# Optimization experiments

Measured on AMD Instinct MI355X. Metric: run time of the kernel, lower is better.

The kernel has to match this reference:

```python
import jax, jax.numpy as jnp
import numpy as np

N, E, IN = 50000, 800000, 128   # nodes, edges, input feature dim
H, C = 8, 32                    # heads, per-head channels
HC = H * C                      # 256 = concat width
NEG_SLOPE = 0.2
BN_EPS = 1e-5


def _gat_conv(x, src, dst, W, a_src, a_dst, b, heads, out_ch, concat):
    """PyG-style GATConv (eval mode, self-loops already in src/dst)."""
    n = x.shape[0]
    h = (x @ W).reshape(n, heads, out_ch)                 # [N,H,C]
    alpha_s = (h * a_src).sum(-1)                         # [N,H]
    alpha_d = (h * a_dst).sum(-1)                         # [N,H]
    e = jax.nn.leaky_relu(alpha_s[src] + alpha_d[dst], NEG_SLOPE)  # [Etot,H]
    # segment softmax over destination nodes (every node has a self-loop)
    emax = jax.ops.segment_max(e, dst, num_segments=n)    # [N,H]
    e = jnp.exp(e - emax[dst])
    denom = jax.ops.segment_sum(e, dst, num_segments=n)
    alpha = e / (denom[dst] + 1e-16)                      # [Etot,H]
    msg = h[src] * alpha[:, :, None]                      # [Etot,H,C]
    out = jax.ops.segment_sum(msg, dst, num_segments=n)   # [N,H,C]
    out = out.reshape(n, heads * out_ch) if concat else out.mean(axis=1)
    return out + b


def _bn(y, g, beta, m, v):
    return (y - m) * jax.lax.rsqrt(v + BN_EPS) * g + beta


def setup_inputs() -> dict:
    key = jax.random.key(0)
    ks = jax.random.split(key, 32)
    def p(i, shape, s=0.1):
        return jax.random.normal(ks[i], shape, dtype=jnp.float32) * s
    x = jax.random.normal(ks[0], (N, IN), dtype=jnp.float32)
    edge_index = jax.random.randint(ks[1], (2, E), 0, N, dtype=jnp.int32)
    d = dict(
        x=x, edge_index=edge_index,
        W1=p(2, (IN, HC)), a_src1=p(3, (H, C)), a_dst1=p(4, (H, C)), b1=p(5, (HC,)),
        bn1_g=jnp.ones((HC,), jnp.float32), bn1_b=jnp.zeros((HC,), jnp.float32),
        bn1_m=p(6, (HC,)), bn1_v=jax.random.uniform(ks[7], (HC,), jnp.float32, 0.5, 1.5),
        W2=p(8, (HC, HC)), a_src2=p(9, (H, C)), a_dst2=p(10, (H, C)), b2=p(11, (HC,)),
        bn2_g=jnp.ones((HC,), jnp.float32), bn2_b=jnp.zeros((HC,), jnp.float32),
        bn2_m=p(12, (HC,)), bn2_v=jax.random.uniform(ks[13], (HC,), jnp.float32, 0.5, 1.5),
        W3=p(14, (HC, C)), a_src3=p(15, (1, C)), a_dst3=p(16, (1, C)), b3=p(17, (C,)),
        Ws1=p(18, (IN, HC)), bs1=p(19, (HC,)),
        Ws2=p(20, (HC, C)), bs2=p(21, (C,)),
    )
    return d


def reference(x, edge_index, W1, a_src1, a_dst1, b1, bn1_g, bn1_b, bn1_m, bn1_v,
              W2, a_src2, a_dst2, b2, bn2_g, bn2_b, bn2_m, bn2_v,
              W3, a_src3, a_dst3, b3, Ws1, bs1, Ws2, bs2):
    n = x.shape[0]
    loops = jnp.arange(n, dtype=edge_index.dtype)
    src = jnp.concatenate([edge_index[0], loops])   # PyG add_self_loops=True
    dst = jnp.concatenate([edge_index[1], loops])
    x0 = x @ Ws1 + bs1                               # skip1
    h = _gat_conv(x, src, dst, W1, a_src1, a_dst1, b1, H, C, True)
    h = jax.nn.elu(_bn(h, bn1_g, bn1_b, bn1_m, bn1_v)) + x0
    xs = h @ Ws2 + bs2                               # skip2
    h2 = _gat_conv(h, src, dst, W2, a_src2, a_dst2, b2, H, C, True)
    h2 = jax.nn.elu(_bn(h2, bn2_g, bn2_b, bn2_m, bn2_v))
    out = _gat_conv(h2, src, dst, W3, a_src3, a_dst3, b3, 1, C, False) + xs
    return out
```

## Files before the change

### kernel.cpp

```cpp
#include <hip/hip_runtime.h>
#include <hip/hip_bf16.h>

#define NEG_SLOPE 0.2f
#define BN_EPS 1e-5f
#define BSH 8
#define STASH_CAP 6400

typedef __attribute__((ext_vector_type(8))) short bf16x8;
typedef __attribute__((ext_vector_type(4))) float f32x4;
typedef __attribute__((ext_vector_type(2))) float f32x2;

#if defined(__has_builtin)
#if __has_builtin(__builtin_amdgcn_cvt_f32_fp8) && __has_builtin(__builtin_amdgcn_cvt_pk_fp8_f32)
#define HW_FP8 1
#endif
#if __has_builtin(__builtin_amdgcn_cvt_pk_f32_fp8)
#define HW_FP8_PK 1
#endif
#endif

__device__ __forceinline__ float bf2f(unsigned short u) {
    union { unsigned int i; float f; } x;
    x.i = ((unsigned int)u) << 16;
    return x.f;
}
__device__ __forceinline__ unsigned short f2bf(float f) {
    __hip_bfloat16 b = __float2bfloat16(f);
    return *reinterpret_cast<unsigned short*>(&b);
}
__device__ __forceinline__ float lrelu(float v) {
    return v > 0.f ? v : NEG_SLOPE * v;
}

__device__ __forceinline__ unsigned char f8enc(float f) {
#ifdef HW_FP8
    int p = __builtin_amdgcn_cvt_pk_fp8_f32(f, 0.f, 0, false);
    return (unsigned char)(p & 0xff);
#else
    float a = fabsf(f);
    unsigned int sign = (__float_as_uint(f) >> 31) << 7;
    if (a < 0.0009765625f) return (unsigned char)sign;
    a = fminf(a, 448.f);
    unsigned int bits = __float_as_uint(a);
    int e = (int)((bits >> 23) & 0xff) - 127;
    unsigned int mant = bits & 0x7fffff;
    if (e < -6) {
        int q = (int)(a * 512.f + 0.5f);
        if (q >= 8) return (unsigned char)(sign | 0x08);
        return (unsigned char)(sign | q);
    }
    unsigned int m = mant >> 20;
    unsigned int rem = mant & 0xfffff;
    if (rem > 0x80000 || (rem == 0x80000 && (m & 1))) m++;
    if (m == 8) { m = 0; e++; }
    if (e > 8) { e = 8; m = 6; }
    return (unsigned char)(sign | ((unsigned int)(e + 7) << 3) | m);
#endif
}
template <int SEL>
__device__ __forceinline__ float f8dec(unsigned int w) {
#ifdef HW_FP8
    return __builtin_amdgcn_cvt_f32_fp8(w, SEL);
#else
    unsigned int b = (w >> (SEL * 8)) & 0xff;
    unsigned int s = b >> 7, em = b & 0x7f;
    float mag;
    if (em >= 8) {
        unsigned int bits = (((em >> 3) + 120) << 23) | ((em & 7) << 20);
        mag = __uint_as_float(bits);
    } else {
        mag = (float)em * 0.001953125f;
    }
    return s ? -mag : mag;
#endif
}
__device__ __forceinline__ void fma_f8x4(float we, unsigned int wv, float4& acc) {
#ifdef HW_FP8_PK
    f32x2 lo = __builtin_amdgcn_cvt_pk_f32_fp8((int)wv, false);
    f32x2 hi = __builtin_amdgcn_cvt_pk_f32_fp8((int)wv, true);
    acc.x = fmaf(we, lo[0], acc.x);
    acc.y = fmaf(we, lo[1], acc.y);
    acc.z = fmaf(we, hi[0], acc.z);
    acc.w = fmaf(we, hi[1], acc.w);
#else
    acc.x = fmaf(we, f8dec<0>(wv), acc.x);
    acc.y = fmaf(we, f8dec<1>(wv), acc.y);
    acc.z = fmaf(we, f8dec<2>(wv), acc.z);
    acc.w = fmaf(we, f8dec<3>(wv), acc.w);
#endif
}

__device__ __forceinline__ int block_scan_incl(int v, int t) {
    int lane = t & 63, w = t >> 6;
    int sv = v;
    #pragma unroll
    for (int off = 1; off < 64; off <<= 1) {
        int u = __shfl_up(sv, off);
        if (lane >= off) sv += u;
    }
    __shared__ int ws_[4];
    if (lane == 63) ws_[w] = sv;
    __syncthreads();
    if (t == 0) {
        int a = 0;
        #pragma unroll
        for (int k = 0; k < 4; k++) { int x = ws_[k]; ws_[k] = a; a += x; }
    }
    __syncthreads();
    return sv + ws_[w];
}

__global__ __launch_bounds__(256) void phase1(const int* __restrict__ dstl,
                                              int E, int N, int NB,
                                              int* __restrict__ gHist,
                                              const float* __restrict__ x,
                                              unsigned short* __restrict__ xb, int n4x,
                                              const float* __restrict__ W1,
                                              const float* __restrict__ Ws1,
                                              const float* __restrict__ W2,
                                              const float* __restrict__ Ws2,
                                              const float* __restrict__ W3,
                                              const float* __restrict__ a_src1,
                                              const float* __restrict__ a_dst1,
                                              const float* __restrict__ a_src2,
                                              const float* __restrict__ a_dst2,
                                              const float* __restrict__ a_src3,
                                              const float* __restrict__ a_dst3,
                                              unsigned short* __restrict__ Wcat1,
                                              unsigned short* __restrict__ Wcat2,
                                              unsigned short* __restrict__ W3t) {
    int t = threadIdx.x;
    if (blockIdx.x < 256) {
        __shared__ int h[256];
        h[t] = 0;
        __syncthreads();
        int Etot = E + N;
        for (int i = blockIdx.x * 256 + t; i < Etot; i += 256 * 256) {
            int d = (i < E) ? dstl[i] : (i - E);
            atomicAdd(&h[d >> BSH], 1);
        }
        __syncthreads();
        if (t < NB && h[t]) atomicAdd(&gHist[t], h[t]);
        return;
    }
    int i = (blockIdx.x - 256) * 256 + t;
    if (i < n4x) {
        float4 v = reinterpret_cast<const float4*>(x)[i];
        ushort4 o;
        o.x = f2bf(v.x); o.y = f2bf(v.y); o.z = f2bf(v.z); o.w = f2bf(v.w);
        reinterpret_cast<ushort4*>(xb)[i] = o;
        return;
    }
    int j = i - n4x;
    if (j < 32768) {
        int m = j >> 7, k = j & 127;
        Wcat1[j] = f2bf(W1[k * 256 + m]);
    } else if (j < 65536) {
        int q = j - 32768; int m = q >> 7, k = q & 127;
        Wcat1[32768 + q] = f2bf(Ws1[k * 256 + m]);
    } else if (j < 131072) {
        int q = j - 65536; int m = q >> 8, k = q & 255;
        Wcat2[q] = f2bf(W2[k * 256 + m]);
    } else if (j < 139264) {
        int q = j - 131072; int m = q >> 8, k = q & 255;
        Wcat2[65536 + q] = f2bf(Ws2[k * 32 + m]);
    } else if (j < 147456) {
        int q = j - 139264; int m = q >> 8, k = q & 255;
        W3t[q] = f2bf(W3[k * 32 + m]);
    } else if (j < 149504) {
        int q = j - 147456; int r = q >> 7, k = q & 127;
        int h = r & 7;
        const float* av = (r < 8) ? a_src1 : a_dst1;
        float s = 0.f;
        #pragma unroll
        for (int c = 0; c < 32; c++) s += W1[k * 256 + h * 32 + c] * av[h * 32 + c];
        Wcat1[(512 + r) * 128 + k] = f2bf(s);
    } else if (j < 153600) {
        int q = j - 149504; int r = q >> 8, k = q & 255;
        int h = r & 7;
        const float* av = (r < 8) ? a_src2 : a_dst2;
        float s = 0.f;
        #pragma unroll
        for (int c = 0; c < 32; c++) s += W2[k * 256 + h * 32 + c] * av[h * 32 + c];
        Wcat2[(288 + r) * 256 + k] = f2bf(s);
    } else if (j < 154112) {
        int q = j - 153600; int r = q >> 8, k = q & 255;
        const float* av = r ? a_dst3 : a_src3;
        float s = 0.f;
        #pragma unroll
        for (int c = 0; c < 32; c++) s += W3[k * 32 + c] * av[c];
        W3t[(32 + r) * 256 + k] = f2bf(s);
    }
}

__global__ __launch_bounds__(256) void bucket_scatter(const int* __restrict__ srcl,
                                                      const int* __restrict__ dstl,
                                                      int E, int N, int NB,
                                                      const int* __restrict__ gHist,
                                                      int* __restrict__ gCursor,
                                                      unsigned int* __restrict__ bktEdges) {
    __shared__ unsigned int stage[4096];
    __shared__ int lbase[256];
    __shared__ int hist[256];
    __shared__ int bexcl[257];
    __shared__ int curk[256];
    __shared__ int gbase[256];
    int t = threadIdx.x;
    int Etot = E + N;
    int begin = blockIdx.x * 4096;

    int gv = (t < NB) ? gHist[t] : 0;
    int gincl = block_scan_incl(gv, t);
    lbase[t] = gincl - gv;
    __syncthreads();

    hist[t] = 0;
    __syncthreads();

    unsigned int ent[16];
    int eb[16];
    #pragma unroll
    for (int k = 0; k < 16; k++) {
        int i = begin + k * 256 + t;
        if (i < Etot) {
            int s, d;
            if (i < E) { s = srcl[i]; d = dstl[i]; }
            else       { s = d = i - E; }
            eb[k] = d >> BSH;
            ent[k] = ((unsigned int)s << BSH) | (unsigned int)(d & 255);
            atomicAdd(&hist[eb[k]], 1);
        } else eb[k] = -1;
    }
    __syncthreads();

    int v = hist[t];
    int incl = block_scan_incl(v, t);
    bexcl[t] = incl - v;
    curk[t] = incl - v;
    if (t == 255) bexcl[256] = incl;
    __syncthreads();

    #pragma unroll
    for (int k = 0; k < 16; k++) {
        if (eb[k] >= 0) {
            int slot = atomicAdd(&curk[eb[k]], 1);
            stage[slot] = ent[k];
        }
    }
    if (t < NB) {
        int cnt = hist[t];
        gbase[t] = cnt ? (lbase[t] + atomicAdd(&gCursor[t], cnt)) : 0;
    }
    __syncthreads();

    int total = bexcl[256];
    for (int p = t; p < total; p += 256) {
        int lo = 0, hi = NB - 1;
        while (lo < hi) {
            int mid = (lo + hi + 1) >> 1;
            if (bexcl[mid] <= p) lo = mid; else hi = mid - 1;
        }
        bktEdges[gbase[lo] + (p - bexcl[lo])] = stage[p];
    }
}

__global__ __launch_bounds__(256) void bucket_to_csr(const unsigned int* __restrict__ bktEdges,
                                                     const int* __restrict__ gHist,
                                                     int* __restrict__ indptr,
                                                     int* __restrict__ esrc,
                                                     int N, int NB, int Etot) {
    __shared__ int lbase[256];
    __shared__ int nh[256];
    __shared__ int ncur[256];
    __shared__ unsigned int stash[STASH_CAP];
    int b = blockIdx.x, t = threadIdx.x;

    int gv = (t < NB) ? gHist[t] : 0;
    int gincl = block_scan_incl(gv, t);
    lbase[t] = gincl - gv;
    __syncthreads();
    int base = lbase[b];
    int cnt = gHist[b];
    int nodeBase = b << BSH;

    nh[t] = 0;
    __syncthreads();
    for (int p = t; p < cnt; p += 256) {
        unsigned int e = bktEdges[base + p];
        if (p < STASH_CAP) stash[p] = e;
        atomicAdd(&nh[e & 255], 1);
    }
    __syncthreads();
    int v = nh[t];
    int incl = block_scan_incl(v, t);
    int excl = incl - v;
    ncur[t] = excl;
    if (nodeBase + t < N) indptr[nodeBase + t] = base + excl;
    __syncthreads();
    for (int p = t; p < cnt; p += 256) {
        unsigned int e = (p < STASH_CAP) ? stash[p] : bktEdges[base + p];
        int slot = atomicAdd(&ncur[e & 255], 1);
        esrc[base + slot] = (int)(e >> BSH);
    }
    if (b == 0 && t == 0) indptr[N] = Etot;
}

__global__ __launch_bounds__(256) void gemm_tile(const unsigned short* __restrict__ A,
                                                 const unsigned short* __restrict__ Bt,
                                                 unsigned short* __restrict__ outBf,
                                                 unsigned char* __restrict__ outQ,
                                                 unsigned short* __restrict__ outSk,
                                                 const float* __restrict__ biasSk,
                                                 float* __restrict__ asOut,
                                                 float* __restrict__ adOut,
                                                 int M, int K, int NCtot,
                                                 int split, int split2,
                                                 int ldBf, int ldSk) {
    int t = threadIdx.x;
    int w = t >> 6, lane = t & 63;
    int l16 = lane & 15, quad = lane >> 4;
    int warp_r = w >> 1, warp_c = w & 1;
    int rowBase = blockIdx.y * 128;
    int colBase = blockIdx.x * 128;

    const unsigned short* aP0; const unsigned short* aP1;
    const unsigned short* aP2; const unsigned short* aP3;
    const unsigned short* bP0; const unsigned short* bP1;
    const unsigned short* bP2; const unsigned short* bP3;
    {
        int r0 = rowBase + warp_r * 64 + 0 * 16 + l16; if (r0 >= M) r0 = M - 1;
        int r1 = rowBase + warp_r * 64 + 1 * 16 + l16; if (r1 >= M) r1 = M - 1;
        int r2 = rowBase + warp_r * 64 + 2 * 16 + l16; if (r2 >= M) r2 = M - 1;
        int r3 = rowBase + warp_r * 64 + 3 * 16 + l16; if (r3 >= M) r3 = M - 1;
        aP0 = A + (size_t)r0 * K + quad * 8;
        aP1 = A + (size_t)r1 * K + quad * 8;
        aP2 = A + (size_t)r2 * K + quad * 8;
        aP3 = A + (size_t)r3 * K + quad * 8;
        int c0 = colBase + warp_c * 64 + 0 * 16 + l16; if (c0 >= NCtot) c0 = NCtot - 1;
        int c1 = colBase + warp_c * 64 + 1 * 16 + l16; if (c1 >= NCtot) c1 = NCtot - 1;
        int c2 = colBase + warp_c * 64 + 2 * 16 + l16; if (c2 >= NCtot) c2 = NCtot - 1;
        int c3 = colBase + warp_c * 64 + 3 * 16 + l16; if (c3 >= NCtot) c3 = NCtot - 1;
        bP0 = Bt + (size_t)c0 * K + quad * 8;
        bP1 = Bt + (size_t)c1 * K + quad * 8;
        bP2 = Bt + (size_t)c2 * K + quad * 8;
        bP3 = Bt + (size_t)c3 * K + quad * 8;
    }

    f32x4 acc[4][4];
    #pragma unroll
    for (int i = 0; i < 4; i++)
        #pragma unroll
        for (int j = 0; j < 4; j++) acc[i][j] = (f32x4){0.f, 0.f, 0.f, 0.f};

    int niter = K >> 5;
    for (int it = 0; it < niter; ++it) {
        int k0 = it << 5;
        bf16x8 a[4], b[4];
        a[0] = *reinterpret_cast<const bf16x8*>(aP0 + k0);
        a[1] = *reinterpret_cast<const bf16x8*>(aP1 + k0);
        a[2] = *reinterpret_cast<const bf16x8*>(aP2 + k0);
        a[3] = *reinterpret_cast<const bf16x8*>(aP3 + k0);
        b[0] = *reinterpret_cast<const bf16x8*>(bP0 + k0);
        b[1] = *reinterpret_cast<const bf16x8*>(bP1 + k0);
        b[2] = *reinterpret_cast<const bf16x8*>(bP2 + k0);
        b[3] = *reinterpret_cast<const bf16x8*>(bP3 + k0);
        #pragma unroll
        for (int i = 0; i < 4; i++)
            #pragma unroll
            for (int j = 0; j < 4; j++)
                acc[i][j] = __builtin_amdgcn_mfma_f32_16x16x32_bf16(a[i], b[j], acc[i][j], 0, 0, 0);
    }

    #pragma unroll
    for (int i = 0; i < 4; i++) {
        #pragma unroll
        for (int r = 0; r < 4; r++) {
            int row = rowBase + warp_r * 64 + i * 16 + quad * 4 + r;
            if (row >= M) continue;
            #pragma unroll
            for (int j = 0; j < 4; j++) {
                int c = colBase + warp_c * 64 + j * 16 + l16;
                if (c >= NCtot) continue;
                float v = acc[i][j][r];
                if (c < split) {
                    if (outBf) outBf[(size_t)row * ldBf + c] = f2bf(v);
                    if (outQ)  outQ[(size_t)row * ldBf + c] = f8enc(v);
                } else if (c < split2) {
                    outSk[(size_t)row * ldSk + (c - split)] = f2bf(v + biasSk[c - split]);
                } else {
                    int a = c - split2;
                    if (NCtot - split2 == 16) {
                        if (a < 8) asOut[(size_t)row * 8 + a] = v;
                        else       adOut[(size_t)row * 8 + a - 8] = v;
                    } else {
                        if (a == 0) asOut[row] = v;
                        else        adOut[row] = v;
                    }
                }
            }
        }
    }
}

template <int MODE>
__global__ __launch_bounds__(256) void agg256(const unsigned char* __restrict__ hq,
                                              const float* __restrict__ as,
                                              const float* __restrict__ ad,
                                              const int* __restrict__ indptr,
                                              const int* __restrict__ esrc,
                                              const float* __restrict__ bias,
                                              const float* __restrict__ bn_g,
                                              const float* __restrict__ bn_b,
                                              const float* __restrict__ bn_m,
                                              const float* __restrict__ bn_v,
                                              const unsigned short* __restrict__ skip,
                                              unsigned short* __restrict__ out, int N) {
    int t = threadIdx.x;
    int n = blockIdx.x * 4 + (t >> 6);
    if (n >= N) return;
    int lane = t & 63;
    int e8 = lane >> 3, h8 = lane & 7;
    int g4 = lane >> 4, cl = lane & 15;
    int hd = cl >> 1;
    int start = indptr[n], end = indptr[n + 1];
    int cnt = end - start;

    float adh = ad[n * 8 + h8];
    const unsigned char* hqc = hq + cl * 16;

    float4 acc0 = make_float4(0.f, 0.f, 0.f, 0.f);
    float4 acc1 = make_float4(0.f, 0.f, 0.f, 0.f);
    float4 acc2 = make_float4(0.f, 0.f, 0.f, 0.f);
    float4 acc3 = make_float4(0.f, 0.f, 0.f, 0.f);
    float sm = 0.f;
    int nfull = cnt & ~7;

    int sA = 0, sB = 0;
    float wA = 0.f, wB = 0.f;
    uint4 hv0 = {}, hv1 = {};
    if (nfull) {
        sA = esrc[start + e8];
        wA = __expf(lrelu(as[sA * 8 + h8] + adh));
        int r0 = __shfl(sA, g4 * 8);
        int r1 = __shfl(sA, (4 + g4) * 8);
        hv0 = *reinterpret_cast<const uint4*>(hqc + (size_t)r0 * 256);
        hv1 = *reinterpret_cast<const uint4*>(hqc + (size_t)r1 * 256);
        if (nfull > 8) {
            sB = esrc[start + 8 + e8];
            wB = __expf(lrelu(as[sB * 8 + h8] + adh));
        }
    }
    for (int i0 = start; i0 < start + nfull; i0 += 8) {
        uint4 u0 = hv0, u1 = hv1;
        float wcur = wA;
        if (i0 + 8 < start + nfull) {
            int r0 = __shfl(sB, g4 * 8);
            int r1 = __shfl(sB, (4 + g4) * 8);
            hv0 = *reinterpret_cast<const uint4*>(hqc + (size_t)r0 * 256);
            hv1 = *reinterpret_cast<const uint4*>(hqc + (size_t)r1 * 256);
        }
        sA = sB; wA = wB;
        if (i0 + 16 < start + nfull) {
            sB = esrc[i0 + 16 + e8];
            wB = __expf(lrelu(as[sB * 8 + h8] + adh));
        }
        sm += wcur;
        float w0 = __shfl(wcur, g4 * 8 + hd);
        float w1 = __shfl(wcur, (4 + g4) * 8 + hd);
        fma_f8x4(w0, u0.x, acc0);
        fma_f8x4(w0, u0.y, acc1);
        fma_f8x4(w0, u0.z, acc2);
        fma_f8x4(w0, u0.w, acc3);
        fma_f8x4(w1, u1.x, acc0);
        fma_f8x4(w1, u1.y, acc1);
        fma_f8x4(w1, u1.z, acc2);
        fma_f8x4(w1, u1.w, acc3);
    }
    int rem = cnt - nfull;
    if (rem) {
        int i0 = start + nfull;
        int idx = i0 + e8;
        bool valid = idx < end;
        int s_r = esrc[valid ? idx : end - 1];
        float w_r = valid ? __expf(lrelu(as[s_r * 8 + h8] + adh)) : 0.f;
        sm += w_r;
        int r0 = __shfl(s_r, g4 * 8);
        uint4 u0 = *reinterpret_cast<const uint4*>(hqc + (size_t)r0 * 256);
        float w0 = __shfl(w_r, g4 * 8 + hd);
        fma_f8x4(w0, u0.x, acc0);
        fma_f8x4(w0, u0.y, acc1);
        fma_f8x4(w0, u0.z, acc2);
        fma_f8x4(w0, u0.w, acc3);
        if (rem > 4) {
            int r1 = __shfl(s_r, (4 + g4) * 8);
            uint4 u1 = *reinterpret_cast<const uint4*>(hqc + (size_t)r1 * 256);
            float w1 = __shfl(w_r, (4 + g4) * 8 + hd);
            fma_f8x4(w1, u1.x, acc0);
            fma_f8x4(w1, u1.y, acc1);
            fma_f8x4(w1, u1.z, acc2);
            fma_f8x4(w1, u1.w, acc3);
        }
    }

    acc0.x += __shfl_xor(acc0.x, 16); acc0.y += __shfl_xor(acc0.y, 16);
    acc0.z += __shfl_xor(acc0.z, 16); acc0.w += __shfl_xor(acc0.w, 16);
    acc0.x += __shfl_xor(acc0.x, 32); acc0.y += __shfl_xor(acc0.y, 32);
    acc0.z += __shfl_xor(acc0.z, 32); acc0.w += __shfl_xor(acc0.w, 32);
    acc1.x += __shfl_xor(acc1.x, 16); acc1.y += __shfl_xor(acc1.y, 16);
    acc1.z += __shfl_xor(acc1.z, 16); acc1.w += __shfl_xor(acc1.w, 16);
    acc1.x += __shfl_xor(acc1.x, 32); acc1.y += __shfl_xor(acc1.y, 32);
    acc1.z += __shfl_xor(acc1.z, 32); acc1.w += __shfl_xor(acc1.w, 32);
    acc2.x += __shfl_xor(acc2.x, 16); acc2.y += __shfl_xor(acc2.y, 16);
    acc2.z += __shfl_xor(acc2.z, 16); acc2.w += __shfl_xor(acc2.w, 16);
    acc2.x += __shfl_xor(acc2.x, 32); acc2.y += __shfl_xor(acc2.y, 32);
    acc2.z += __shfl_xor(acc2.z, 32); acc2.w += __shfl_xor(acc2.w, 32);
    acc3.x += __shfl_xor(acc3.x, 16); acc3.y += __shfl_xor(acc3.y, 16);
    acc3.z += __shfl_xor(acc3.z, 16); acc3.w += __shfl_xor(acc3.w, 16);
    acc3.x += __shfl_xor(acc3.x, 32); acc3.y += __shfl_xor(acc3.y, 32);
    acc3.z += __shfl_xor(acc3.z, 32); acc3.w += __shfl_xor(acc3.w, 32);

    #pragma unroll
    for (int off = 8; off < 64; off <<= 1) sm += __shfl_xor(sm, off);
    float il = 1.f / (sm + 1e-16f);
    float il_c = __shfl(il, hd);

    float4 my;
    if (g4 == 0)      my = acc0;
    else if (g4 == 1) my = acc1;
    else if (g4 == 2) my = acc2;
    else              my = acc3;
    int cb = cl * 16 + g4 * 4;

    float4 bv  = *reinterpret_cast<const float4*>(&bias[cb]);
    float4 gv  = *reinterpret_cast<const float4*>(&bn_g[cb]);
    float4 bbv = *reinterpret_cast<const float4*>(&bn_b[cb]);
    float4 mv  = *reinterpret_cast<const float4*>(&bn_m[cb]);
    float4 vv  = *reinterpret_cast<const float4*>(&bn_v[cb]);
    float o[4] = {my.x * il_c + bv.x, my.y * il_c + bv.y,
                  my.z * il_c + bv.z, my.w * il_c + bv.w};
    float g[4] = {gv.x, gv.y, gv.z, gv.w}, bb[4] = {bbv.x, bbv.y, bbv.z, bbv.w};
    float m[4] = {mv.x, mv.y, mv.z, mv.w}, vr[4] = {vv.x, vv.y, vv.z, vv.w};
    float sk[4] = {0.f, 0.f, 0.f, 0.f};
    if (MODE == 1) {
        ushort4 s4 = *reinterpret_cast<const ushort4*>(&skip[(size_t)n * 256 + cb]);
        sk[0] = bf2f(s4.x); sk[1] = bf2f(s4.y); sk[2] = bf2f(s4.z); sk[3] = bf2f(s4.w);
    }
    ushort4 res;
    unsigned short* rp = &res.x;
    #pragma unroll
    for (int j = 0; j < 4; j++) {
        float val = (o[j] - m[j]) * rsqrtf(vr[j] + BN_EPS) * g[j] + bb[j];
        val = val > 0.f ? val : (__expf(val) - 1.f);
        val += sk[j];
        rp[j] = f2bf(val);
    }
    *reinterpret_cast<ushort4*>(&out[(size_t)n * 256 + cb]) = res;
}

__global__ __launch_bounds__(256) void agg32(const unsigned short* __restrict__ h3,
                                             const float* __restrict__ as,
                                             const float* __restrict__ ad,
                                             const int* __restrict__ indptr,
                                             const int* __restrict__ esrc,
                                             const float* __restrict__ b3,
                                             const unsigned short* __restrict__ xs,
                                             float* __restrict__ out, int N) {
    int t = threadIdx.x;
    int n = blockIdx.x * 4 + (t >> 6);
    if (n >= N) return;
    int lane = t & 63;
    int e_sub = lane >> 3, c4 = (lane & 7) * 4;
    int start = indptr[n], end = indptr[n + 1];
    float adn = ad[n];

    float4 acc = make_float4(0.f, 0.f, 0.f, 0.f);
    float sm = 0.f;
    int i0 = start;
    for (; i0 + 16 <= end; i0 += 16) {
        int sA = esrc[i0 + e_sub];
        int sB = esrc[i0 + 8 + e_sub];
        float wA = __expf(lrelu(as[sA] + adn));
        float wB = __expf(lrelu(as[sB] + adn));
        sm += wA + wB;
        ushort4 hA = *reinterpret_cast<const ushort4*>(&h3[(size_t)sA * 32 + c4]);
        ushort4 hB = *reinterpret_cast<const ushort4*>(&h3[(size_t)sB * 32 + c4]);
        acc.x = fmaf(wA, bf2f(hA.x), acc.x); acc.y = fmaf(wA, bf2f(hA.y), acc.y);
        acc.z = fmaf(wA, bf2f(hA.z), acc.z); acc.w = fmaf(wA, bf2f(hA.w), acc.w);
        acc.x = fmaf(wB, bf2f(hB.x), acc.x); acc.y = fmaf(wB, bf2f(hB.y), acc.y);
        acc.z = fmaf(wB, bf2f(hB.z), acc.z); acc.w = fmaf(wB, bf2f(hB.w), acc.w);
    }
    for (; i0 < end; i0 += 8) {
        int idx = i0 + e_sub;
        bool valid = idx < end;
        if (valid) {
            int s = esrc[idx];
            float w = __expf(lrelu(as[s] + adn));
            sm += w;
            ushort4 hv = *reinterpret_cast<const ushort4*>(&h3[(size_t)s * 32 + c4]);
            acc.x = fmaf(w, bf2f(hv.x), acc.x);
            acc.y = fmaf(w, bf2f(hv.y), acc.y);
            acc.z = fmaf(w, bf2f(hv.z), acc.z);
            acc.w = fmaf(w, bf2f(hv.w), acc.w);
        }
    }
    #pragma unroll
    for (int off = 8; off < 64; off <<= 1) {
        sm    += __shfl_xor(sm, off);
        acc.x += __shfl_xor(acc.x, off);
        acc.y += __shfl_xor(acc.y, off);
        acc.z += __shfl_xor(acc.z, off);
        acc.w += __shfl_xor(acc.w, off);
    }
    if (e_sub == 0) {
        float il = 1.f / (sm + 1e-16f);
        float4 bv = *reinterpret_cast<const float4*>(&b3[c4]);
        ushort4 xv = *reinterpret_cast<const ushort4*>(&xs[(size_t)n * 32 + c4]);
        float4 o;
        o.x = acc.x * il + bv.x + bf2f(xv.x);
        o.y = acc.y * il + bv.y + bf2f(xv.y);
        o.z = acc.z * il + bv.z + bf2f(xv.z);
        o.w = acc.w * il + bv.w + bf2f(xv.w);
        *reinterpret_cast<float4*>(&out[(size_t)n * 32 + c4]) = o;
    }
}

extern "C" void kernel_launch(void* const* d_in, const int* in_sizes, int n_in,
                              void* d_out, int out_size, void* d_ws, size_t ws_size,
                              hipStream_t stream) {
    const float* x      = (const float*)d_in[0];
    const int*   eidx   = (const int*)  d_in[1];
    const float* W1     = (const float*)d_in[2];
    const float* a_src1 = (const float*)d_in[3];
    const float* a_dst1 = (const float*)d_in[4];
    const float* b1     = (const float*)d_in[5];
    const float* bn1_g  = (const float*)d_in[6];
    const float* bn1_b  = (const float*)d_in[7];
    const float* bn1_m  = (const float*)d_in[8];
    const float* bn1_v  = (const float*)d_in[9];
    const float* W2     = (const float*)d_in[10];
    const float* a_src2 = (const float*)d_in[11];
    const float* a_dst2 = (const float*)d_in[12];
    const float* b2     = (const float*)d_in[13];
    const float* bn2_g  = (const float*)d_in[14];
    const float* bn2_b  = (const float*)d_in[15];
    const float* bn2_m  = (const float*)d_in[16];
    const float* bn2_v  = (const float*)d_in[17];
    const float* W3     = (const float*)d_in[18];
    const float* a_src3 = (const float*)d_in[19];
    const float* a_dst3 = (const float*)d_in[20];
    const float* b3     = (const float*)d_in[21];
    const float* Ws1    = (const float*)d_in[22];
    const float* bs1    = (const float*)d_in[23];
    const float* Ws2    = (const float*)d_in[24];
    const float* bs2    = (const float*)d_in[25];

    const int N = in_sizes[0] / 128;
    const int E = in_sizes[1] / 2;
    const int Etot = E + N;
    const int NB = (N + 255) >> 8;
    const int* srcl = eidx;
    const int* dstl = eidx + E;

    char* ws = (char*)d_ws;
    size_t off = 0;
    auto alloc = [&](size_t bytes) -> void* {
        void* p = ws + off;
        off += (bytes + 255) & ~(size_t)255;
        return p;
    };
    unsigned short* xb    = (unsigned short*)alloc((size_t)N * 128 * 2);
    unsigned short* feat  = (unsigned short*)alloc((size_t)N * 256 * 2);
    unsigned char*  hq    = (unsigned char*)alloc((size_t)N * 256);
    unsigned short* h2b   = (unsigned short*)alloc((size_t)N * 256 * 2);
    unsigned short* featb = (unsigned short*)alloc((size_t)N * 256 * 2);
    unsigned short* xsbuf = (unsigned short*)alloc((size_t)N * 32 * 2);
    unsigned short* h3b   = (unsigned short*)alloc((size_t)N * 32 * 2);
    float*          asb   = (float*)alloc((size_t)N * 8 * 4);
    float*          adb   = (float*)alloc((size_t)N * 8 * 4);
    unsigned short* Wcat1 = (unsigned short*)alloc((size_t)528 * 128 * 2);
    unsigned short* Wcat2 = (unsigned short*)alloc((size_t)304 * 256 * 2);
    unsigned short* W3t   = (unsigned short*)alloc((size_t)34 * 256 * 2);
    int* gHC     = (int*)alloc(512 * 4);
    int* gHist   = gHC;
    int* gCursor = gHC + 256;
    unsigned int* bktEdges = (unsigned int*)alloc((size_t)Etot * 4);
    int* indptr  = (int*)alloc((size_t)(N + 1) * 4);
    int* esrc    = (int*)alloc((size_t)Etot * 4);
    (void)ws_size; (void)n_in; (void)out_size;

    hipMemsetAsync(gHC, 0, 512 * 4, stream);
    int n4x = N * 128 / 4;
    int prepBlocks = (n4x + 154112 + 255) / 256;
    phase1<<<256 + prepBlocks, 256, 0, stream>>>(dstl, E, N, NB, gHist,
                                                 x, xb, n4x,
                                                 W1, Ws1, W2, Ws2, W3,
                                                 a_src1, a_dst1, a_src2, a_dst2,
                                                 a_src3, a_dst3,
                                                 Wcat1, Wcat2, W3t);
    bucket_scatter<<<(Etot + 4095) / 4096, 256, 0, stream>>>(srcl, dstl, E, N, NB,
                                                             gHist, gCursor, bktEdges);
    bucket_to_csr<<<NB, 256, 0, stream>>>(bktEdges, gHist, indptr, esrc, N, NB, Etot);

    int gy128 = (N + 127) / 128;
    int gn4 = (N + 3) / 4;

    gemm_tile<<<dim3(5, gy128), 256, 0, stream>>>(xb, Wcat1, nullptr, hq, feat, bs1,
                                                  asb, adb,
                                                  N, 128, 528, 256, 512, 256, 256);
    agg256<1><<<gn4, 256, 0, stream>>>(hq, asb, adb, indptr, esrc, b1,
                                       bn1_g, bn1_b, bn1_m, bn1_v, feat, h2b, N);

    gemm_tile<<<dim3(3, gy128), 256, 0, stream>>>(h2b, Wcat2, nullptr, hq, xsbuf, bs2,
                                                  asb, adb,
                                                  N, 256, 304, 256, 288, 256, 32);
    agg256<0><<<gn4, 256, 0, stream>>>(hq, asb, adb, indptr, esrc, b2,
                                       bn2_g, bn2_b, bn2_m, bn2_v, nullptr, featb, N);

    gemm_tile<<<dim3(1, gy128), 256, 0, stream>>>(featb, W3t, h3b, nullptr, nullptr, nullptr,
                                                  asb, adb,
                                                  N, 256, 34, 32, 32, 32, 32);
    agg32<<<gn4, 256, 0, stream>>>(h3b, asb, adb, indptr, esrc, b3, xsbuf,
                                   (float*)d_out, N);
}
```

Baseline: 401.9 us.

## Replace 2D-tiled GEMM with row-panel GEMM keeping A in registers

After: 479.3 us. 19.3% more time.

```diff
diff --git a/kernel.cpp b/kernel.cpp
--- a/kernel.cpp
+++ b/kernel.cpp
@@ -305,90 +305,78 @@
     if (b == 0 && t == 0) indptr[N] = Etot;
 }
 
-__global__ __launch_bounds__(256) void gemm_tile(const unsigned short* __restrict__ A,
-                                                 const unsigned short* __restrict__ Bt,
-                                                 unsigned short* __restrict__ outBf,
-                                                 unsigned char* __restrict__ outQ,
-                                                 unsigned short* __restrict__ outSk,
-                                                 const float* __restrict__ biasSk,
-                                                 float* __restrict__ asOut,
-                                                 float* __restrict__ adOut,
-                                                 int M, int K, int NCtot,
-                                                 int split, int split2,
-                                                 int ldBf, int ldSk) {
+template <int K>
+__global__ __launch_bounds__(256) void gemm_panel(const unsigned short* __restrict__ A,
+                                                  const unsigned short* __restrict__ Bt,
+                                                  unsigned short* __restrict__ outBf,
+                                                  unsigned char* __restrict__ outQ,
+                                                  unsigned short* __restrict__ outSk,
+                                                  const float* __restrict__ biasSk,
+                                                  float* __restrict__ asOut,
+                                                  float* __restrict__ adOut,
+                                                  int M, int NCtot,
+                                                  int split, int split2,
+                                                  int ldBf, int ldSk) {
+    constexpr int KS = K / 32;
     int t = threadIdx.x;
     int w = t >> 6, lane = t & 63;
     int l16 = lane & 15, quad = lane >> 4;
-    int warp_r = w >> 1, warp_c = w & 1;
-    int rowBase = blockIdx.y * 128;
-    int colBase = blockIdx.x * 128;
-
-    const unsigned short* aP0; const unsigned short* aP1;
-    const unsigned short* aP2; const unsigned short* aP3;
-    const unsigned short* bP0; const unsigned short* bP1;
-    const unsigned short* bP2; const unsigned short* bP3;
+    int rowBase = blockIdx.x * 64 + w * 16;
+
+    bf16x8 af[KS];
     {
-        int r0 = rowBase + warp_r * 64 + 0 * 16 + l16; if (r0 >= M) r0 = M - 1;
-        int r1 = rowBase + warp_r * 64 + 1 * 16 + l16; if (r1 >= M) r1 = M - 1;
-        int r2 = rowBase + warp_r * 64 + 2 * 16 + l16; if (r2 >= M) r2 = M - 1;
-        int r3 = rowBase + warp_r * 64 + 3 * 16 + l16; if (r3 >= M) r3 = M - 1;
-        aP0 = A + (size_t)r0 * K + quad * 8;
-        aP1 = A + (size_t)r1 * K + quad * 8;
-        aP2 = A + (size_t)r2 * K + quad * 8;
-        aP3 = A + (size_t)r3 * K + quad * 8;
-        int c0 = colBase + warp_c * 64 + 0 * 16 + l16; if (c0 >= NCtot) c0 = NCtot - 1;
-        int c1 = colBase + warp_c * 64 + 1 * 16 + l16; if (c1 >= NCtot) c1 = NCtot - 1;
-        int c2 = colBase + warp_c * 64 + 2 * 16 + l16; if (c2 >= NCtot) c2 = NCtot - 1;
-        int c3 = colBase + warp_c * 64 + 3 * 16 + l16; if (c3 >= NCtot) c3 = NCtot - 1;
-        bP0 = Bt + (size_t)c0 * K + quad * 8;
-        bP1 = Bt + (size_t)c1 * K + quad * 8;
-        bP2 = Bt + (size_t)c2 * K + quad * 8;
-        bP3 = Bt + (size_t)c3 * K + quad * 8;
-    }
-
-    f32x4 acc[4][4];
-    #pragma unroll
-    for (int i = 0; i < 4; i++)
+        int gr = rowBase + l16; if (gr >= M) gr = M - 1;
+        const unsigned short* aP = A + (size_t)gr * K + quad * 8;
         #pragma unroll
-        for (int j = 0; j < 4; j++) acc[i][j] = (f32x4){0.f, 0.f, 0.f, 0.f};
-
-    int niter = K >> 5;
-    for (int it = 0; it < niter; ++it) {
-        int k0 = it << 5;
-        bf16x8 a[4], b[4];
-        a[0] = *reinterpret_cast<const bf16x8*>(aP0 + k0);
-        a[1] = *reinterpret_cast<const bf16x8*>(aP1 + k0);
-        a[2] = *reinterpret_cast<const bf16x8*>(aP2 + k0);
-        a[3] = *reinterpret_cast<const bf16x8*>(aP3 + k0);
-        b[0] = *reinterpret_cast<const bf16x8*>(bP0 + k0);
-        b[1] = *reinterpret_cast<const bf16x8*>(bP1 + k0);
-        b[2] = *reinterpret_cast<const bf16x8*>(bP2 + k0);
-        b[3] = *reinterpret_cast<const bf16x8*>(bP3 + k0);
+        for (int ks = 0; ks < KS; ks++)
+            af[ks] = *reinterpret_cast<const bf16x8*>(aP + ks * 32);
+    }
+
+    for (int colBase = 0; colBase < NCtot; colBase += 128) {
+        f32x4 acc[8];
         #pragma unroll
-        for (int i = 0; i < 4; i++)
+        for (int j = 0; j < 8; j++) acc[j] = (f32x4){0.f, 0.f, 0.f, 0.f};
+
+        #pragma unroll
+        for (int j = 0; j < 8; j++) {
+            int cc = colBase + j * 16 + l16;
+            if (cc >= NCtot) cc = NCtot - 1;
+            const unsigned short* bP = Bt + (size_t)cc * K + quad * 8;
             #pragma unroll
-            for (int j = 0; j < 4; j++)
-                acc[i][j] = __builtin_amdgcn_mfma_f32_16x16x32_bf16(a[i], b[j], acc[i][j], 0, 0, 0);
-    }
-
-    #pragma unroll
-    for (int i = 0; i < 4; i++) {
+            for (int ks = 0; ks < KS; ks++) {
+                bf16x8 b = *reinterpret_cast<const bf16x8*>(bP + ks * 32);
+                acc[j] = __builtin_amdgcn_mfma_f32_16x16x32_bf16(af[ks], b, acc[j], 0, 0, 0);
+            }
+        }
+
         #pragma unroll
-        for (int r = 0; r < 4; r++) {
-            int row = rowBase + warp_r * 64 + i * 16 + quad * 4 + r;
-            if (row >= M) continue;
-            #pragma unroll
-            for (int j = 0; j < 4; j++) {
-                int c = colBase + warp_c * 64 + j * 16 + l16;
-                if (c >= NCtot) continue;
-                float v = acc[i][j][r];
-                if (c < split) {
+        for (int j = 0; j < 8; j++) {
+            int c = colBase + j * 16 + l16;
+            if (c >= NCtot) continue;
+            if (c < split) {
+                #pragma unroll
+                for (int r = 0; r < 4; r++) {
+                    int row = rowBase + quad * 4 + r;
+                    if (row >= M) continue;
+                    float v = acc[j][r];
                     if (outBf) outBf[(size_t)row * ldBf + c] = f2bf(v);
                     if (outQ)  outQ[(size_t)row * ldBf + c] = f8enc(v);
-                } else if (c < split2) {
-                    outSk[(size_t)row * ldSk + (c - split)] = f2bf(v + biasSk[c - split]);
-                } else {
-                    int a = c - split2;
+                }
+            } else if (c < split2) {
+                float bv = biasSk[c - split];
+                #pragma unroll
+                for (int r = 0; r < 4; r++) {
+                    int row = rowBase + quad * 4 + r;
+                    if (row >= M) continue;
+                    outSk[(size_t)row * ldSk + (c - split)] = f2bf(acc[j][r] + bv);
+                }
+            } else {
+                int a = c - split2;
+                #pragma unroll
+                for (int r = 0; r < 4; r++) {
+                    int row = rowBase + quad * 4 + r;
+                    if (row >= M) continue;
+                    float v = acc[j][r];
                     if (NCtot - split2 == 16) {
                         if (a < 8) asOut[(size_t)row * 8 + a] = v;
                         else       adOut[(size_t)row * 8 + a - 8] = v;
@@ -701,24 +689,24 @@
                                                              gHist, gCursor, bktEdges);
     bucket_to_csr<<<NB, 256, 0, stream>>>(bktEdges, gHist, indptr, esrc, N, NB, Etot);
 
-    int gy128 = (N + 127) / 128;
+    int gy64 = (N + 63) / 64;
     int gn4 = (N + 3) / 4;
 
-    gemm_tile<<<dim3(5, gy128), 256, 0, stream>>>(xb, Wcat1, nullptr, hq, feat, bs1,
-                                                  asb, adb,
-                                                  N, 128, 528, 256, 512, 256, 256);
+    gemm_panel<128><<<gy64, 256, 0, stream>>>(xb, Wcat1, nullptr, hq, feat, bs1,
+                                              asb, adb,
+                                              N, 528, 256, 512, 256, 256);
     agg256<1><<<gn4, 256, 0, stream>>>(hq, asb, adb, indptr, esrc, b1,
                                        bn1_g, bn1_b, bn1_m, bn1_v, feat, h2b, N);
 
-    gemm_tile<<<dim3(3, gy128), 256, 0, stream>>>(h2b, Wcat2, nullptr, hq, xsbuf, bs2,
-                                                  asb, adb,
-                                                  N, 256, 304, 256, 288, 256, 32);
+    gemm_panel<256><<<gy64, 256, 0, stream>>>(h2b, Wcat2, nullptr, hq, xsbuf, bs2,
+                                              asb, adb,
+                                              N, 304, 256, 288, 256, 32);
     agg256<0><<<gn4, 256, 0, stream>>>(hq, asb, adb, indptr, esrc, b2,
                                        bn2_g, bn2_b, bn2_m, bn2_v, nullptr, featb, N);
 
-    gemm_tile<<<dim3(1, gy128), 256, 0, stream>>>(featb, W3t, h3b, nullptr, nullptr, nullptr,
-                                                  asb, adb,
-                                                  N, 256, 34, 32, 32, 32, 32);
+    gemm_panel<256><<<gy64, 256, 0, stream>>>(featb, W3t, h3b, nullptr, nullptr, nullptr,
+                                              asb, adb,
+                                              N, 34, 32, 32, 32, 32);
     agg32<<<gn4, 256, 0, stream>>>(h3b, asb, adb, indptr, esrc, b3, xsbuf,
                                    (float*)d_out, N);
 }
```
